# Kernel optimization log

Measured on AMD Instinct MI355X. Metric: run time of the kernel, lower is better.

## Reference

```python
import jax, jax.numpy as jnp
import numpy as np

BSZ, SL, D, K, K_U, K_Y, SCALE = 4, 2048, 256, 24, 3, 2, 4
H = SCALE * D


def _hankel(n):
    i = np.arange(1, n + 1, dtype=np.float64)
    s = i[:, None] + i[None, :]
    return 2.0 / (s ** 3 - s)


def setup_inputs() -> dict:
    key = jax.random.key(0)
    ks = jax.random.split(key, 9)
    Z = _hankel(SL)
    ev, evec = np.linalg.eigh(Z)  # ascending
    sigma = jnp.asarray(np.clip(ev[-K:], 1e-12, None), jnp.float32)  # (K,)
    phi = jnp.asarray(evec[:, -K:], jnp.float32)  # (SL, K) top-k eigenvectors
    s = 0.02
    return {
        'x': jax.random.normal(ks[0], (BSZ, SL, D), jnp.float32),
        'sigma': sigma,
        'phi': phi,
        'rms_w': jnp.ones((D,), jnp.float32),
        'M_u': jax.random.normal(ks[1], (K_U, D, D), jnp.float32) * s,
        'M_phi_plus': jax.random.normal(ks[2], (K, D, D), jnp.float32) * s,
        'M_phi_minus': jax.random.normal(ks[3], (K, D, D), jnp.float32) * s,
        'm_y': jax.random.normal(ks[4], (K_Y, D, D), jnp.float32) * s,
        'w1': jax.random.normal(ks[5], (D, H), jnp.float32) * s,
        'v': jax.random.normal(ks[6], (D, H), jnp.float32) * s,
        'w2': jax.random.normal(ks[7], (H, D), jnp.float32) * s,
    }


def _rmsnorm(x, w, eps=1e-6):
    return x * jax.lax.rsqrt(jnp.mean(x * x, axis=-1, keepdims=True) + eps) * w


def _shift(u, i):
    # causal time shift: out[:, t] = u[:, t-i], zero-padded
    if i == 0:
        return u
    return jnp.pad(u, ((0, 0), (i, 0), (0, 0)))[:, :-i, :]


def _causal_conv(phi, u):
    # U[b,t,k,d] = sum_{s<=t} phi[s,k] * u[b,t-s,d], via FFT (linear conv, length 2*sl)
    sl = u.shape[1]
    n = 2 * sl
    Fu = jnp.fft.rfft(u, n=n, axis=1)  # (b, nf, d)
    Fp = jnp.fft.rfft(phi, n=n, axis=0)  # (nf, k)
    prod = Fu[:, :, None, :] * Fp[None, :, :, None]  # (b, nf, k, d)
    return jnp.fft.irfft(prod, n=n, axis=1)[:, :sl]  # (b, sl, k, d)


def _stu(u, sigma, phi, M_u, M_phi_plus, M_phi_minus, m_y):
    k_u = M_u.shape[0]
    ar_u = sum(jnp.einsum('btd,od->bto', _shift(u, i), M_u[i]) for i in range(k_u))
    # spectral term: eigenfilter causal convolutions on u and alternating-sign u
    alt = jnp.where(jnp.arange(u.shape[1]) % 2 == 0, 1.0, -1.0)[None, :, None]
    Up = _causal_conv(phi, u)
    Um = _causal_conv(phi, u * alt)
    sr = sigma ** 0.25
    spectral = (jnp.einsum('btkd,k,kod->bto', Up, sr, M_phi_plus)
                + jnp.einsum('btkd,k,kod->bto', Um, sr, M_phi_minus))
    y = ar_u + spectral  # (b, sl, d)
    # sequential AR recurrence over outputs: yhat_t = y_t + sum_i m_y[i] @ yhat_{t-1-i}
    k_y, d = m_y.shape[0], m_y.shape[2]
    b = u.shape[0]

    def step(carry, y_t):  # carry: (k_y, b, d), most recent first
        ar = jnp.einsum('kod,kbd->bo', m_y, carry)
        yhat = y_t + ar
        carry = jnp.concatenate([yhat[None], carry[:-1]], axis=0)
        return carry, ar

    carry0 = jnp.zeros((k_y, b, d), u.dtype)
    _, ar_y = jax.lax.scan(step, carry0, jnp.swapaxes(y, 0, 1))
    return y + jnp.swapaxes(ar_y, 0, 1)


def reference(x, sigma, phi, rms_w, M_u, M_phi_plus, M_phi_minus, m_y, w1, v, w2):
    z = x
    h = _stu(_rmsnorm(x, rms_w), sigma, phi, M_u, M_phi_plus, M_phi_minus, m_y)
    mlp = (jax.nn.silu(h @ w1) * (h @ v)) @ w2  # SwiGLU
    h = h + mlp
    return h + z
```

## Files before the change

kernel.cpp:

```cpp
#include <hip/hip_runtime.h>
#include <hip/hip_bf16.h>
#include <math.h>

#define SLEN 2048
#define DIM 256
#define NB 4
#define NKF 24
#define NH 1024
#define NROW (NB*SLEN)
#define NTOT (NB*SLEN*DIM)

#define BM 128
#define BN 256
#define BKK 32
#define PADK 40

#define KG 3
#define KPB 8
#define VELEMS ((size_t)NKF*NB*DIM*SLEN)

typedef __attribute__((ext_vector_type(8))) short bf16x8;
typedef __attribute__((ext_vector_type(4))) float f32x4;

struct __align__(16) U4 { unsigned int a, b, c, d; };
struct __align__(8)  S4 { unsigned short x, y, z, w; };

__device__ __forceinline__ unsigned short f2b(float v){
    union { __hip_bfloat16 h; unsigned short u; } cv;
    cv.h = __float2bfloat16(v);
    return cv.u;
}
__device__ __forceinline__ float b2f(unsigned short s){
    union { __hip_bfloat16 h; unsigned short u; } cv;
    cv.u = s;
    return __bfloat162float(cv.h);
}

__device__ __forceinline__ void gl_lds(const unsigned short* g, unsigned short* l){
    __builtin_amdgcn_global_load_lds((const __attribute__((address_space(1))) void*)g,
                                     (__attribute__((address_space(3))) void*)l, 16, 0, 0);
}

__device__ __forceinline__ int swzS(int row, int g){
    return ((row >> 3) << 5) + (g << 3) + ((row & 7) ^ g);
}

__global__ void k_prep(const float4* __restrict__ Mu, const float4* __restrict__ Mp,
                       const float4* __restrict__ Mm,
                       const float* __restrict__ w1, const float* __restrict__ vv,
                       const float* __restrict__ w2, const float* __restrict__ my,
                       const float* __restrict__ phi,
                       S4* __restrict__ MuB, S4* __restrict__ MpB, S4* __restrict__ MmB,
                       unsigned short* __restrict__ w1T, unsigned short* __restrict__ vT,
                       unsigned short* __restrict__ w2T,
                       unsigned short* __restrict__ pw, unsigned short* __restrict__ pwTs,
                       unsigned short* __restrict__ Q, unsigned short* __restrict__ Tt){
    int bid = blockIdx.x, tix = threadIdx.x;
    if (bid < 192){
        int i = bid*256 + tix;
        float4 v = Mu[i];
        S4 p; p.x=f2b(v.x); p.y=f2b(v.y); p.z=f2b(v.z); p.w=f2b(v.w);
        MuB[i] = p; return;
    }
    bid -= 192;
    if (bid < 1536){
        int i = bid*256 + tix;
        float4 v = Mp[i];
        S4 p; p.x=f2b(v.x); p.y=f2b(v.y); p.z=f2b(v.z); p.w=f2b(v.w);
        MpB[i] = p; return;
    }
    bid -= 1536;
    if (bid < 1536){
        int i = bid*256 + tix;
        float4 v = Mm[i];
        S4 p; p.x=f2b(v.x); p.y=f2b(v.y); p.z=f2b(v.z); p.w=f2b(v.w);
        MmB[i] = p; return;
    }
    bid -= 1536;
    if (bid < 1024){
        int i = bid*256 + tix; int r = i >> 10, c = i & 1023;
        w1T[(size_t)c*DIM + r] = f2b(w1[i]); return;
    }
    bid -= 1024;
    if (bid < 1024){
        int i = bid*256 + tix; int r = i >> 10, c = i & 1023;
        vT[(size_t)c*DIM + r] = f2b(vv[i]); return;
    }
    bid -= 1024;
    if (bid < 1024){
        int i = bid*256 + tix; int r = i >> 8, c = i & 255;
        w2T[(size_t)c*NH + r] = f2b(w2[i]); return;
    }
    bid -= 1024;
    if (bid < 1024){
        int i = bid*256 + tix;
        int r = i >> 9, c = i & 511;
        float v;
        if (r < 256) v = (c < 256) ? my[r*256 + c] : my[256*256 + r*256 + (c - 256)];
        else         v = (c == r - 256) ? 1.0f : 0.0f;
        unsigned short bb = f2b(v);
        pw [262144 + (size_t)r*512 + c] = bb;
        pwTs[(size_t)c*512 + r] = bb;
        if (r < 256 && c < 256) Q[65536 + r*256 + c] = bb;
        return;
    }
    bid -= 1024;
    {
        int i = bid*256 + tix;
        int e   = (i & 7) * 4;
        int row = (i >> 3) & 127;
        int c   = (i >> 10) & 7;
        int rem = (i >> 13) & 15;
        int k   = i >> 17;
        int d0 = rem*128 + row - (c*32 + e);
        S4 p;
        p.x = (d0   >= 0) ? f2b(phi[(size_t)(d0  )*NKF + k]) : (unsigned short)0;
        p.y = (d0-1 >= 0) ? f2b(phi[(size_t)(d0-1)*NKF + k]) : (unsigned short)0;
        p.z = (d0-2 >= 0) ? f2b(phi[(size_t)(d0-2)*NKF + k]) : (unsigned short)0;
        p.w = (d0-3 >= 0) ? f2b(phi[(size_t)(d0-3)*NKF + k]) : (unsigned short)0;
        size_t base = ((size_t)((k*16 + rem)*8 + c)) * 4096;
        *(S4*)&Tt[base + swzS(row, e>>3)*8 + (e&7)] = p;
    }
}

__global__ void k_rmsnorm(const float* __restrict__ x, const float* __restrict__ w, unsigned short* __restrict__ u){
    int row = blockIdx.x;
    int t = threadIdx.x;
    float v = x[(size_t)row*DIM + t];
    float ss = v*v;
    #pragma unroll
    for (int o = 32; o > 0; o >>= 1) ss += __shfl_down(ss, o, 64);
    __shared__ float red[4];
    if ((t & 63) == 0) red[t >> 6] = ss;
    __syncthreads();
    float tot = red[0]+red[1]+red[2]+red[3];
    float sc = rsqrtf(tot * (1.0f/256.0f) + 1e-6f);
    u[(size_t)row*DIM + t] = f2b(v * sc * w[t]);
}

__global__ void k_prep2(const float4* __restrict__ y, float4* __restrict__ out, S4* __restrict__ ybf){
    int i = blockIdx.x*256 + threadIdx.x;
    if (i < NTOT/4){
        float4 v = y[i];
        out[i] = v;
        S4 p; p.x=f2b(v.x); p.y=f2b(v.y); p.z=f2b(v.z); p.w=f2b(v.w);
        ybf[i] = p;
    }
}


__device__ __forceinline__ void mfma_tile(const unsigned short* Al, const unsigned short* Bl,
                                          f32x4 acc[4][4], int lane, int wr, int wc){
    int cl = lane & 15;
    int kb = (lane >> 4) * 8;
    bf16x8 a[4], b[4];
    #pragma unroll
    for (int mi = 0; mi < 4; ++mi)
        a[mi] = *(const bf16x8*)&Al[(wr*64 + mi*16 + cl)*PADK + kb];
    #pragma unroll
    for (int ni = 0; ni < 4; ++ni)
        b[ni] = *(const bf16x8*)&Bl[(wc*64 + ni*16 + cl)*PADK + kb];
    #pragma unroll
    for (int mi = 0; mi < 4; ++mi)
        #pragma unroll
        for (int ni = 0; ni < 4; ++ni)
            acc[mi][ni] = __builtin_amdgcn_mfma_f32_16x16x32_bf16(a[mi], b[ni], acc[mi][ni], 0, 0, 0);
}

#define GEMM_PROLOG \
    __shared__ unsigned short Al[BM*PADK]; \
    __shared__ unsigned short Bl[BN*PADK]; \
    int tid = threadIdx.x, lane = tid & 63, wv = tid >> 6, wr = wv >> 2, wc = wv & 3; \
    f32x4 acc[4][4]; \
    { f32x4 z = {0.f,0.f,0.f,0.f}; \
      for (int mi=0;mi<4;++mi) for (int ni=0;ni<4;++ni) acc[mi][ni] = z; }

__global__ __launch_bounds__(512) void k_pow(unsigned short* __restrict__ pw, unsigned short* __restrict__ pwTs,
                                             unsigned short* __restrict__ Q, int s, int ns){
    int mt = blockIdx.x, nt = blockIdx.y;
    int j = 1 + blockIdx.z;
    int p = ns + j;
    int m0 = mt * BM, n0 = nt * BN;
    if (p > 16 && (m0 >= 256 || n0 >= 256)) return;
    GEMM_PROLOG
    const unsigned short* A = pw   + (size_t)j * 262144;
    const unsigned short* B = pwTs + (size_t)s * 262144;
    for (int k0 = 0; k0 < 512; k0 += BKK){
        __syncthreads();
        { int row = tid >> 2, sg = tid & 3;
          *(U4*)&Al[row*PADK + sg*8] = *(const U4*)&A[(size_t)(m0+row)*512 + k0 + sg*8]; }
        #pragma unroll
        for (int ss = 0; ss < 2; ++ss){ int q = tid + ss*512; int row = q >> 2, sg = q & 3;
          *(U4*)&Bl[row*PADK + sg*8] = *(const U4*)&B[(size_t)(n0+row)*512 + k0 + sg*8]; }
        __syncthreads();
        mfma_tile(Al, Bl, acc, lane, wr, wc);
    }
    int cl = lane & 15, rg = (lane >> 4) * 4;
    #pragma unroll
    for (int mi=0; mi<4; ++mi){
        int rb = m0 + wr*64 + mi*16 + rg;
        #pragma unroll
        for (int ni=0; ni<4; ++ni){
            int col = n0 + wc*64 + ni*16 + cl;
            unsigned short bb[4];
            #pragma unroll
            for (int r=0;r<4;++r) bb[r] = f2b(acc[mi][ni][r]);
            if (p <= 16){
                #pragma unroll
                for (int r=0;r<4;++r) pw[(size_t)p*262144 + (size_t)(rb+r)*512 + col] = bb[r];
            }
            if (j == ns && ns <= 8){
                S4 pk; pk.x=bb[0]; pk.y=bb[1]; pk.z=bb[2]; pk.w=bb[3];
                *(S4*)&pwTs[(size_t)(s+1)*262144 + (size_t)col*512 + rb] = pk;
            }
            if (rb < 256 && col < 256){
                #pragma unroll
                for (int r=0;r<4;++r) Q[(size_t)p*65536 + (size_t)(rb+r)*256 + col] = bb[r];
            }
        }
    }
}

__global__ __launch_bounds__(512) void k_aru(const unsigned short* __restrict__ u,
                                             const unsigned short* __restrict__ Mu, float* __restrict__ y){
    GEMM_PROLOG
    int tt = blockIdx.x, b = blockIdx.y;
    int t0 = tt * BM;
    const unsigned short* Ab = u + (size_t)b*SLEN*DIM;
    for (int i = 0; i < 3; ++i){
        const unsigned short* Bsrc = Mu + (size_t)i*65536;
        for (int k0 = 0; k0 < 256; k0 += BKK){
            __syncthreads();
            { int row = tid >> 2, sg = tid & 3; int t = t0 + row - i;
              U4 val; val.a=val.b=val.c=val.d=0u;
              if (t >= 0) val = *(const U4*)&Ab[(size_t)t*DIM + k0 + sg*8];
              *(U4*)&Al[row*PADK + sg*8] = val; }
            #pragma unroll
            for (int s = 0; s < 2; ++s){ int q = tid + s*512; int row = q >> 2, sg = q & 3;
              *(U4*)&Bl[row*PADK + sg*8] = *(const U4*)&Bsrc[(size_t)row*DIM + k0 + sg*8]; }
            __syncthreads();
            mfma_tile(Al, Bl, acc, lane, wr, wc);
        }
    }
    int cl = lane & 15, rg = (lane >> 4) * 4;
    #pragma unroll
    for (int mi=0; mi<4; ++mi){
        int tb = t0 + wr*64 + mi*16 + rg;
        #pragma unroll
        for (int ni=0; ni<4; ++ni){
            int o = wc*64 + ni*16 + cl;
            #pragma unroll
            for (int r=0;r<4;++r) y[((size_t)b*SLEN + tb + r)*DIM + o] = acc[mi][ni][r];
        }
    }
}

__global__ __launch_bounds__(512) void k_proj(const unsigned short* __restrict__ u,
                                              const unsigned short* __restrict__ Mp,
                                              const unsigned short* __restrict__ Mm,
                                              const float* __restrict__ sigma,
                                              unsigned short* __restrict__ V){
    __shared__ unsigned short Al[BM*PADK];
    __shared__ unsigned short Bl0[BN*PADK];
    __shared__ unsigned short Bl1[BN*PADK];
    int tid = threadIdx.x, lane = tid & 63, wv = tid >> 6, wr = wv >> 2, wc = wv & 3;
    f32x4 acc0[4][4], acc1[4][4];
    { f32x4 z = {0.f,0.f,0.f,0.f};
      for (int mi=0;mi<4;++mi) for (int ni=0;ni<4;++ni){ acc0[mi][ni] = z; acc1[mi][ni] = z; } }
    int tt = blockIdx.x, b = blockIdx.y, k = blockIdx.z;
    int t0 = tt * BM;
    float sr = powf(sigma[k], 0.25f);
    const unsigned short* Asrc  = u + ((size_t)b*SLEN + t0)*DIM;
    const unsigned short* B0src = Mp + (size_t)k*65536;
    const unsigned short* B1src = Mm + (size_t)k*65536;
    for (int k0 = 0; k0 < 256; k0 += BKK){
        __syncthreads();
        { int row = tid >> 2, sg = tid & 3;
          *(U4*)&Al[row*PADK + sg*8] = *(const U4*)&Asrc[(size_t)row*DIM + k0 + sg*8]; }
        #pragma unroll
        for (int s = 0; s < 2; ++s){ int q = tid + s*512; int row = q >> 2, sg = q & 3;
          *(U4*)&Bl0[row*PADK + sg*8] = *(const U4*)&B0src[(size_t)row*DIM + k0 + sg*8];
          *(U4*)&Bl1[row*PADK + sg*8] = *(const U4*)&B1src[(size_t)row*DIM + k0 + sg*8]; }
        __syncthreads();
        mfma_tile(Al, Bl0, acc0, lane, wr, wc);
        mfma_tile(Al, Bl1, acc1, lane, wr, wc);
    }
    int cl = lane & 15, rg = (lane >> 4) * 4;
    unsigned short* Tr = Bl0;
    const int TRS = 136;
    #pragma unroll
    for (int ps = 0; ps < 4; ++ps){
        __syncthreads();
        if (wc == ps){
            #pragma unroll
            for (int mi=0; mi<4; ++mi){
                int tl = wr*64 + mi*16 + rg;
                #pragma unroll
                for (int ni=0; ni<4; ++ni){
                    int ol = ni*16 + cl;
                    S4 pk;
                    float s0 = ((t0+tl+0)&1) ? -1.0f : 1.0f;
                    float s1 = ((t0+tl+1)&1) ? -1.0f : 1.0f;
                    float s2 = ((t0+tl+2)&1) ? -1.0f : 1.0f;
                    float s3 = ((t0+tl+3)&1) ? -1.0f : 1.0f;
                    pk.x = f2b(sr*(acc0[mi][ni][0] + s0*acc1[mi][ni][0]));
                    pk.y = f2b(sr*(acc0[mi][ni][1] + s1*acc1[mi][ni][1]));
                    pk.z = f2b(sr*(acc0[mi][ni][2] + s2*acc1[mi][ni][2]));
                    pk.w = f2b(sr*(acc0[mi][ni][3] + s3*acc1[mi][ni][3]));
                    *(S4*)&Tr[ol*TRS + tl] = pk;
                }
            }
        }
        __syncthreads();
        { int row = tid >> 3, seg = tid & 7;
          U4 v0 = *(const U4*)&Tr[row*TRS + seg*16];
          U4 v1 = *(const U4*)&Tr[row*TRS + seg*16 + 8];
          int o  = ps*64 + row;
          int tb = (t0 >> 5) + (seg >> 1);
          int g0 = (seg & 1) * 2;
          size_t sb = ((size_t)(k*NB + b)*64 + tb) * 8192;
          *(U4*)&V[sb + swzS(o, g0  )*8] = v0;
          *(U4*)&V[sb + swzS(o, g0+1)*8] = v1; }
    }
}

__global__ __launch_bounds__(512) void k_conv(const unsigned short* __restrict__ V,
                                              const unsigned short* __restrict__ Tt,
                                              float* __restrict__ y){
    __shared__ __align__(16) unsigned short Abuf[2][4096];
    __shared__ __align__(16) unsigned short Bbuf[2][8192];
    int tid = threadIdx.x, lane = tid & 63, wv = tid >> 6, wr = wv >> 2, wc = wv & 3;
    f32x4 acc[4][4];
    { f32x4 z = {0.f,0.f,0.f,0.f};
      for (int mi=0;mi<4;++mi) for (int ni=0;ni<4;++ni) acc[mi][ni] = z; }

    int b = blockIdx.y, kg = blockIdx.z;
    int px0 = blockIdx.x;
    int px = (px0 & 7)*9 + (px0 >> 3);
    int jx = 0, rem = px;
    #pragma unroll
    for (int j = 0; j < 8; ++j){
        int c = 16 - 2*j;
        if (rem < c){ jx = j; break; }
        rem -= c;
    }
    int tt = 2*jx + rem;
    int t0 = tt*BM;
    int cl = lane & 15, g = lane >> 4;

    int aoff[4], boff[4];
    #pragma unroll
    for (int mi = 0; mi < 4; ++mi) aoff[mi] = swzS(wr*64 + mi*16 + cl, g) << 4;
    #pragma unroll
    for (int ni = 0; ni < 4; ++ni) boff[ni] = swzS(wc*64 + ni*16 + cl, g) << 4;

    auto stage = [&](int bi, int step){
        int kk = step >> 3, ts = step & 7;
        int k = kg*KPB + kk;
        const unsigned short* As = Tt + ((size_t)((k*16 + rem)*8 + ts))*4096 + wv*512;
        const unsigned short* Bs = V  + (((size_t)(k*NB + b)*64 + jx*8 + ts))*8192 + wv*1024;
        gl_lds(As + lane*8,       &Abuf[bi][wv*512]);
        gl_lds(Bs + lane*8,       &Bbuf[bi][wv*1024]);
        gl_lds(Bs + 512 + lane*8, &Bbuf[bi][wv*1024 + 512]);
    };

    stage(0, 0);
    __syncthreads();
    int cur = 0;
    for (int step = 0; step < KPB*8; ++step){
        if (step < KPB*8 - 1) stage(cur^1, step+1);
        bf16x8 a[4], bb[4];
        #pragma unroll
        for (int mi = 0; mi < 4; ++mi)
            a[mi] = *(const bf16x8*)((const char*)Abuf[cur] + aoff[mi]);
        #pragma unroll
        for (int ni = 0; ni < 4; ++ni)
            bb[ni] = *(const bf16x8*)((const char*)Bbuf[cur] + boff[ni]);
        #pragma unroll
        for (int mi = 0; mi < 4; ++mi)
            #pragma unroll
            for (int ni = 0; ni < 4; ++ni)
                acc[mi][ni] = __builtin_amdgcn_mfma_f32_16x16x32_bf16(a[mi], bb[ni], acc[mi][ni], 0, 0, 0);
        __syncthreads();
        cur ^= 1;
    }
    int rg = (lane >> 4) * 4;
    #pragma unroll
    for (int mi=0; mi<4; ++mi){
        int tb = t0 + wr*64 + mi*16 + rg;
        #pragma unroll
        for (int ni=0; ni<4; ++ni){
            int o = wc*64 + ni*16 + cl;
            #pragma unroll
            for (int r=0;r<4;++r) atomicAdd(&y[((size_t)b*SLEN + tb + r)*DIM + o], acc[mi][ni][r]);
        }
    }
}

__global__ __launch_bounds__(512) void k_qconv(const unsigned short* __restrict__ ybf,
                                               const unsigned short* __restrict__ Q,
                                               float* __restrict__ yh){
    GEMM_PROLOG
    int tt = blockIdx.x, b = blockIdx.y, gz = blockIdx.z;
    int t0 = tt * BM;
    const unsigned short* ysrc = ybf + (size_t)b*SLEN*DIM;
    for (int pi = 0; pi < 8; ++pi){
        int p = gz*8 + pi;
        if (p == 0) continue;
        const unsigned short* Qp = Q + (size_t)p*65536;
        for (int k0 = 0; k0 < 256; k0 += BKK){
            __syncthreads();
            { int row = tid >> 2, sg = tid & 3; int t = t0 + row - p;
              U4 val; val.a=val.b=val.c=val.d=0u;
              if (t >= 0) val = *(const U4*)&ysrc[(size_t)t*DIM + k0 + sg*8];
              *(U4*)&Al[row*PADK + sg*8] = val; }
            #pragma unroll
            for (int s = 0; s < 2; ++s){ int q = tid + s*512; int row = q >> 2, sg = q & 3;
              *(U4*)&Bl[row*PADK + sg*8] = *(const U4*)&Qp[(size_t)row*256 + k0 + sg*8]; }
            __syncthreads();
            mfma_tile(Al, Bl, acc, lane, wr, wc);
        }
    }
    int cl = lane & 15, rg = (lane >> 4) * 4;
    #pragma unroll
    for (int mi=0; mi<4; ++mi){
        int tb = t0 + wr*64 + mi*16 + rg;
        #pragma unroll
        for (int ni=0; ni<4; ++ni){
            int o = wc*64 + ni*16 + cl;
            #pragma unroll
            for (int r=0;r<4;++r) atomicAdd(&yh[((size_t)b*SLEN + tb + r)*DIM + o], acc[mi][ni][r]);
        }
    }
}

__global__ __launch_bounds__(512) void k_mlp1f(const float* __restrict__ yhat,
                                               const unsigned short* __restrict__ w1T,
                                               const unsigned short* __restrict__ vT,
                                               unsigned short* __restrict__ act){
    __shared__ unsigned short Al[BM*PADK];
    __shared__ unsigned short Bl0[BN*PADK];
    __shared__ unsigned short Bl1[BN*PADK];
    int tid = threadIdx.x, lane = tid & 63, wv = tid >> 6, wr = wv >> 2, wc = wv & 3;
    f32x4 acc0[4][4], acc1[4][4];
    { f32x4 z = {0.f,0.f,0.f,0.f};
      for (int mi=0;mi<4;++mi) for (int ni=0;ni<4;++ni){ acc0[mi][ni] = z; acc1[mi][ni] = z; } }
    int tt = blockIdx.x, b = blockIdx.y, nt = blockIdx.z;
    int t0 = tt * BM, h0 = nt * 256;
    const float* Asrc = yhat + ((size_t)b*SLEN + t0)*DIM;
    const unsigned short* B0src = w1T + (size_t)h0*DIM;
    const unsigned short* B1src = vT  + (size_t)h0*DIM;
    for (int k0 = 0; k0 < 256; k0 += BKK){
        __syncthreads();
        { int row = tid >> 2, sg = tid & 3;
          const float* src = &Asrc[(size_t)row*DIM + k0 + sg*8];
          float4 f0 = *(const float4*)src, f1 = *(const float4*)(src+4);
          union { U4 v; unsigned short s[8]; } pk;
          pk.s[0]=f2b(f0.x); pk.s[1]=f2b(f0.y); pk.s[2]=f2b(f0.z); pk.s[3]=f2b(f0.w);
          pk.s[4]=f2b(f1.x); pk.s[5]=f2b(f1.y); pk.s[6]=f2b(f1.z); pk.s[7]=f2b(f1.w);
          *(U4*)&Al[row*PADK + sg*8] = pk.v; }
        #pragma unroll
        for (int s = 0; s < 2; ++s){ int q = tid + s*512; int row = q >> 2, sg = q & 3;
          *(U4*)&Bl0[row*PADK + sg*8] = *(const U4*)&B0src[(size_t)row*DIM + k0 + sg*8];
          *(U4*)&Bl1[row*PADK + sg*8] = *(const U4*)&B1src[(size_t)row*DIM + k0 + sg*8]; }
        __syncthreads();
        mfma_tile(Al, Bl0, acc0, lane, wr, wc);
        mfma_tile(Al, Bl1, acc1, lane, wr, wc);
    }
    int cl = lane & 15, rg = (lane >> 4) * 4;
    #pragma unroll
    for (int mi=0; mi<4; ++mi){
        int tb = t0 + wr*64 + mi*16 + rg;
        #pragma unroll
        for (int ni=0; ni<4; ++ni){
            int h = h0 + wc*64 + ni*16 + cl;
            #pragma unroll
            for (int r=0; r<4; ++r){
                float av = acc0[mi][ni][r];
                float sv = av / (1.0f + expf(-av));
                act[(size_t)(b*SLEN + tb + r)*NH + h] = f2b(sv * acc1[mi][ni][r]);
            }
        }
    }
}

__global__ __launch_bounds__(512) void k_mlp2(const unsigned short* __restrict__ act,
                                              const unsigned short* __restrict__ w2T,
                                              const float* __restrict__ x,
                                              float* __restrict__ out){
    GEMM_PROLOG
    int tt = blockIdx.x, b = blockIdx.y, ks = blockIdx.z;
    int t0 = tt * BM;
    size_t bt0 = (size_t)b*SLEN + t0;
    for (int k0 = ks*256; k0 < ks*256 + 256; k0 += BKK){
        __syncthreads();
        { int row = tid >> 2, sg = tid & 3;
          *(U4*)&Al[row*PADK + sg*8] = *(const U4*)&act[(bt0 + row)*NH + k0 + sg*8]; }
        #pragma unroll
        for (int s = 0; s < 2; ++s){ int q = tid + s*512; int row = q >> 2, sg = q & 3;
          *(U4*)&Bl[row*PADK + sg*8] = *(const U4*)&w2T[(size_t)row*NH + k0 + sg*8]; }
        __syncthreads();
        mfma_tile(Al, Bl, acc, lane, wr, wc);
    }
    int cl = lane & 15, rg = (lane >> 4) * 4;
    #pragma unroll
    for (int mi=0; mi<4; ++mi){
        #pragma unroll
        for (int ni=0; ni<4; ++ni){
            int o = wc*64 + ni*16 + cl;
            #pragma unroll
            for (int r=0;r<4;++r){
                size_t idx = (bt0 + wr*64 + mi*16 + rg + r)*DIM + o;
                float add = acc[mi][ni][r] + (ks == 0 ? x[idx] : 0.0f);
                atomicAdd(&out[idx], add);
            }
        }
    }
}


extern "C" void kernel_launch(void* const* d_in, const int* in_sizes, int n_in,
                              void* d_out, int out_size, void* d_ws, size_t ws_size,
                              hipStream_t stream) {
    (void)in_sizes; (void)n_in; (void)out_size;
    const float* x     = (const float*)d_in[0];
    const float* sigma = (const float*)d_in[1];
    const float* phi   = (const float*)d_in[2];
    const float* rmsw  = (const float*)d_in[3];
    const float* Mu    = (const float*)d_in[4];
    const float* Mp    = (const float*)d_in[5];
    const float* Mm    = (const float*)d_in[6];
    const float* my    = (const float*)d_in[7];
    const float* w1    = (const float*)d_in[8];
    const float* vv    = (const float*)d_in[9];
    const float* w2    = (const float*)d_in[10];
    float* out = (float*)d_out;

    char* ws = (char*)d_ws;
    size_t off = 0;
    auto alloc = [&](size_t bytes){ size_t o = off; off += (bytes + 255) & ~(size_t)255; return o; };

    size_t o_u    = alloc((size_t)NROW*DIM*2);
    size_t o_T    = alloc((size_t)NKF*16*128*256*2);
    size_t o_MuB  = alloc((size_t)3*65536*2);
    size_t o_MpB  = alloc((size_t)NKF*65536*2);
    size_t o_MmB  = alloc((size_t)NKF*65536*2);
    size_t o_w1T  = alloc((size_t)NH*DIM*2);
    size_t o_vT   = alloc((size_t)NH*DIM*2);
    size_t o_w2T  = alloc((size_t)DIM*NH*2);
    size_t o_pow  = alloc((size_t)17*262144*2);
    size_t o_powT = alloc((size_t)6*262144*2);
    size_t o_Q    = alloc((size_t)32*65536*2);
    size_t o_y    = alloc((size_t)NTOT*4);
    size_t o_ybf  = alloc((size_t)NTOT*2);
    size_t o_V    = alloc(VELEMS*2);
    if (off > ws_size) return;

    unsigned short* u_b  = (unsigned short*)(ws + o_u);
    unsigned short* Tt   = (unsigned short*)(ws + o_T);
    unsigned short* MuB  = (unsigned short*)(ws + o_MuB);
    unsigned short* MpB  = (unsigned short*)(ws + o_MpB);
    unsigned short* MmB  = (unsigned short*)(ws + o_MmB);
    unsigned short* w1T  = (unsigned short*)(ws + o_w1T);
    unsigned short* vT   = (unsigned short*)(ws + o_vT);
    unsigned short* w2T  = (unsigned short*)(ws + o_w2T);
    unsigned short* pw   = (unsigned short*)(ws + o_pow);
    unsigned short* pwTs = (unsigned short*)(ws + o_powT);
    unsigned short* Q    = (unsigned short*)(ws + o_Q);
    float* y             = (float*)(ws + o_y);
    unsigned short* ybf  = (unsigned short*)(ws + o_ybf);
    unsigned short* V    = (unsigned short*)(ws + o_V);
    unsigned short* act  = (unsigned short*)(ws + o_V);

    k_prep<<<dim3(19648), 256, 0, stream>>>((const float4*)Mu, (const float4*)Mp, (const float4*)Mm,
                                            w1, vv, w2, my, phi,
                                            (S4*)MuB, (S4*)MpB, (S4*)MmB,
                                            w1T, vT, w2T, pw, pwTs, Q, Tt);

    k_rmsnorm<<<dim3(NROW), 256, 0, stream>>>(x, rmsw, u_b);

    const int ns[5]   = {1, 2, 4, 8, 16};
    const int cnts[5] = {1, 2, 4, 8, 15};
    for (int s = 0; s < 5; ++s)
        k_pow<<<dim3(4, 2, cnts[s]), 512, 0, stream>>>(pw, pwTs, Q, s, ns[s]);

    k_aru<<<dim3(16, NB), 512, 0, stream>>>(u_b, MuB, y);

    k_proj<<<dim3(16, NB, NKF), 512, 0, stream>>>(u_b, MpB, MmB, sigma, V);
    k_conv<<<dim3(72, NB, KG), 512, 0, stream>>>(V, Tt, y);

    k_prep2<<<dim3(NTOT/4/256), 256, 0, stream>>>((const float4*)y, (float4*)out, (S4*)ybf);

    k_qconv<<<dim3(16, NB, 4), 512, 0, stream>>>(ybf, Q, out);

    k_mlp1f<<<dim3(16, NB, 4), 512, 0, stream>>>(out, w1T, vT, act);
    k_mlp2<<<dim3(16, NB, 4), 512, 0, stream>>>(act, w2T, x, out);
}
```

Measured before the change: 551.3 us.

## Triple-buffer k_conv LDS pipeline and split k_qconv over more blocks

The causal-conv GEMM moves from a double-buffered loop with a full __syncthreads to a three-stage LDS ring. It uses explicit vmcnt waits and raw s_barrier, so two global-to-LDS loads stay in flight while one buffer is computed. Separately, k_qconv halves the number of lag matrices each block handles and doubles the grid z dimension to expose more parallelism. The ring raises LDS use per block, which may cut occupancy, and the hand-written waitcnt/barrier ordering is fragile.

```diff
diff --git a/kernel.cpp b/kernel.cpp
--- a/kernel.cpp
+++ b/kernel.cpp
@@ -327,8 +327,8 @@
 __global__ __launch_bounds__(512) void k_conv(const unsigned short* __restrict__ V,
                                               const unsigned short* __restrict__ Tt,
                                               float* __restrict__ y){
-    __shared__ __align__(16) unsigned short Abuf[2][4096];
-    __shared__ __align__(16) unsigned short Bbuf[2][8192];
+    __shared__ __align__(16) unsigned short Abuf[3][4096];
+    __shared__ __align__(16) unsigned short Bbuf[3][8192];
     int tid = threadIdx.x, lane = tid & 63, wv = tid >> 6, wr = wv >> 2, wc = wv & 3;
     f32x4 acc[4][4];
     { f32x4 z = {0.f,0.f,0.f,0.f};
@@ -354,36 +354,52 @@
     #pragma unroll
     for (int ni = 0; ni < 4; ++ni) boff[ni] = swzS(wc*64 + ni*16 + cl, g) << 4;
 
+    const unsigned short* Abase = Tt + (size_t)((kg*KPB*16 + rem)*8) * 4096;
+    const unsigned short* Bbase = V  + (((size_t)(kg*KPB*NB + b)*64 + jx*8)) * 8192;
+
     auto stage = [&](int bi, int step){
         int kk = step >> 3, ts = step & 7;
-        int k = kg*KPB + kk;
-        const unsigned short* As = Tt + ((size_t)((k*16 + rem)*8 + ts))*4096 + wv*512;
-        const unsigned short* Bs = V  + (((size_t)(k*NB + b)*64 + jx*8 + ts))*8192 + wv*1024;
+        const unsigned short* As = Abase + ((size_t)kk*16*8 + ts)*4096 + wv*512;
+        const unsigned short* Bs = Bbase + ((size_t)kk*NB*64 + ts)*8192 + wv*1024;
         gl_lds(As + lane*8,       &Abuf[bi][wv*512]);
         gl_lds(Bs + lane*8,       &Bbuf[bi][wv*1024]);
         gl_lds(Bs + 512 + lane*8, &Bbuf[bi][wv*1024 + 512]);
     };
 
-    stage(0, 0);
-    __syncthreads();
-    int cur = 0;
-    for (int step = 0; step < KPB*8; ++step){
-        if (step < KPB*8 - 1) stage(cur^1, step+1);
+    auto compute = [&](int bi){
         bf16x8 a[4], bb[4];
         #pragma unroll
         for (int mi = 0; mi < 4; ++mi)
-            a[mi] = *(const bf16x8*)((const char*)Abuf[cur] + aoff[mi]);
+            a[mi] = *(const bf16x8*)((const char*)Abuf[bi] + aoff[mi]);
         #pragma unroll
         for (int ni = 0; ni < 4; ++ni)
-            bb[ni] = *(const bf16x8*)((const char*)Bbuf[cur] + boff[ni]);
+            bb[ni] = *(const bf16x8*)((const char*)Bbuf[bi] + boff[ni]);
         #pragma unroll
         for (int mi = 0; mi < 4; ++mi)
             #pragma unroll
             for (int ni = 0; ni < 4; ++ni)
                 acc[mi][ni] = __builtin_amdgcn_mfma_f32_16x16x32_bf16(a[mi], bb[ni], acc[mi][ni], 0, 0, 0);
-        __syncthreads();
-        cur ^= 1;
-    }
+    };
+
+    stage(0, 0);
+    stage(1, 1);
+    int cur = 0;
+    for (int t = 0; t < KPB*8 - 1; ++t){
+        asm volatile("s_waitcnt vmcnt(3)" ::: "memory");
+        __builtin_amdgcn_s_barrier();
+        __builtin_amdgcn_sched_barrier(0);
+        compute(cur);
+        if (t + 2 < KPB*8){
+            int nb = cur + 2; if (nb >= 3) nb -= 3;
+            stage(nb, t + 2);
+        }
+        cur = (cur == 2) ? 0 : cur + 1;
+    }
+    asm volatile("s_waitcnt vmcnt(0)" ::: "memory");
+    __builtin_amdgcn_s_barrier();
+    __builtin_amdgcn_sched_barrier(0);
+    compute(cur);
+
     int rg = (lane >> 4) * 4;
     #pragma unroll
     for (int mi=0; mi<4; ++mi){
@@ -404,8 +420,8 @@
     int tt = blockIdx.x, b = blockIdx.y, gz = blockIdx.z;
     int t0 = tt * BM;
     const unsigned short* ysrc = ybf + (size_t)b*SLEN*DIM;
-    for (int pi = 0; pi < 8; ++pi){
-        int p = gz*8 + pi;
+    for (int pi = 0; pi < 4; ++pi){
+        int p = gz*4 + pi;
         if (p == 0) continue;
         const unsigned short* Qp = Q + (size_t)p*65536;
         for (int k0 = 0; k0 < 256; k0 += BKK){
@@ -591,7 +607,7 @@
 
     k_prep2<<<dim3(NTOT/4/256), 256, 0, stream>>>((const float4*)y, (float4*)out, (S4*)ybf);
 
-    k_qconv<<<dim3(16, NB, 4), 512, 0, stream>>>(ybf, Q, out);
+    k_qconv<<<dim3(16, NB, 8), 512, 0, stream>>>(ybf, Q, out);
 
     k_mlp1f<<<dim3(16, NB, 4), 512, 0, stream>>>(out, w1T, vT, act);
     k_mlp2<<<dim3(16, NB, 4), 512, 0, stream>>>(act, w2T, x, out);
```

Measured after the change: 547.0 us. No clear change (-0.8%).
